# Performance work log

Hardware: AMD Instinct MI355X
Metric: run time of the kernel (lower is better)

## Reference

```python
import jax, jax.numpy as jnp
import numpy as np

NUM_GROUPS = 32
EPS = 1e-5


def group_norm(x, scale, bias):
    # x: [b, c, h, w]
    b, c, h, w = x.shape
    xg = x.reshape(b, NUM_GROUPS, c // NUM_GROUPS, h, w)
    mean = jnp.mean(xg, axis=(2, 3, 4), keepdims=True)
    var = jnp.var(xg, axis=(2, 3, 4), keepdims=True)
    xg = (xg - mean) * jax.lax.rsqrt(var + EPS)
    xn = xg.reshape(b, c, h, w)
    return xn * scale[None, :, None, None] + bias[None, :, None, None]


def conv1x1(x, w, b):
    # x: [b, c_in, h, w], w: [c_out, c_in], b: [c_out]
    return jnp.einsum('bchw,dc->bdhw', x, w) + b[None, :, None, None]


def setup_inputs() -> dict:
    key = jax.random.key(0)
    ks = jax.random.split(key, 11)
    B, C, H, W = 16, 512, 32, 32
    s = 1.0 / np.sqrt(C)
    inp = {
        'x': jax.random.normal(ks[0], (B, C, H, W), jnp.float32),
        'gn_scale': jnp.ones((C,), jnp.float32),
        'gn_bias': jnp.zeros((C,), jnp.float32),
        'wq': jax.random.normal(ks[1], (C, C), jnp.float32) * s,
        'bq': jnp.zeros((C,), jnp.float32),
        'wk': jax.random.normal(ks[2], (C, C), jnp.float32) * s,
        'bk': jnp.zeros((C,), jnp.float32),
        'wv': jax.random.normal(ks[3], (C, C), jnp.float32) * s,
        'bv': jnp.zeros((C,), jnp.float32),
        'wp': jax.random.normal(ks[4], (C, C), jnp.float32) * s,
        'bp': jnp.zeros((C,), jnp.float32),
    }
    return inp


def reference(x, gn_scale, gn_bias, wq, bq, wk, bk, wv, bv, wp, bp):
    b, c, h, w = x.shape
    xn = group_norm(x, gn_scale, gn_bias)
    q = conv1x1(xn, wq, bq).reshape(b, c, h * w)  # [b, c, n]
    k = conv1x1(xn, wk, bk).reshape(b, c, h * w)
    v = conv1x1(xn, wv, bv).reshape(b, c, h * w)
    # attn[b, i, j] = sum_c q[b, c, i] * k[b, c, j]
    attn = jnp.einsum('bci,bcj->bij', q, k) * (c ** -0.5)
    A = jax.nn.softmax(attn, axis=-1)
    # out[b, c, i] = sum_j A[b, i, j] * v[b, c, j]
    out = jnp.einsum('bij,bcj->bci', A, v).reshape(b, c, h, w)
    scores = conv1x1(out, wp, bp)
    return x + scores
```

## Files before the change

kernel.cpp:

```cpp
#include <hip/hip_runtime.h>

typedef __bf16 bf16x8 __attribute__((ext_vector_type(8)));
typedef float  f32x4  __attribute__((ext_vector_type(4)));

__device__ __forceinline__ unsigned short f2bf(float f) {
    union { float f; unsigned int u; } x; x.f = f;
    unsigned int r = (x.u + 0x7FFFu + ((x.u >> 16) & 1u)) >> 16;
    return (unsigned short)r;
}

typedef const __attribute__((address_space(1))) unsigned short gu16;
typedef __attribute__((address_space(3)))       unsigned short lu16;
__device__ __forceinline__ void gl_lds16(const unsigned short* g, unsigned short* l) {
    __builtin_amdgcn_global_load_lds((gu16*)g, (lu16*)l, 16, 0, 0);
}

__device__ __forceinline__ void stage_tiles(
    const unsigned short* __restrict__ Ab, int lda,
    const unsigned short* __restrict__ Bb, int ldb,
    int k0, unsigned short* Ad, unsigned short* Bd,
    int wave, int r0, int c0)
{
    gl_lds16(Ab + (long)r0 * lda + c0 + k0,        Ad + wave * 512);
    gl_lds16(Ab + (long)(r0 + 64) * lda + c0 + k0, Ad + 2048 + wave * 512);
    gl_lds16(Bb + (long)r0 * ldb + c0 + k0,        Bd + wave * 512);
    gl_lds16(Bb + (long)(r0 + 64) * ldb + c0 + k0, Bd + 2048 + wave * 512);
}

__device__ __forceinline__ void gemm_core_db(
    const unsigned short* __restrict__ Ab, int lda,
    const unsigned short* __restrict__ Bb, int ldb,
    int K, f32x4 (&acc)[4][4],
    unsigned short* As, unsigned short* Bs)
{
    const int tid  = threadIdx.x;
    const int lane = tid & 63;
    const int wave = tid >> 6;
    const int wm   = (wave >> 1) * 64;
    const int wn   = (wave & 1) * 64;
    const int l16  = lane & 15;
    const int quad = lane >> 4;

    const int r0 = wave * 16 + (lane >> 2);
    const int c0 = ((lane & 3) ^ ((lane >> 3) & 3)) * 8;

    stage_tiles(Ab, lda, Bb, ldb, 0, As, Bs, wave, r0, c0);

    const int sw8 = ((l16 >> 1) & 3) * 8;

    int sel = 0;
    for (int k0 = 0; k0 < K; k0 += 32) {
        __syncthreads();
        if (k0 + 32 < K)
            stage_tiles(Ab, lda, Bb, ldb, k0 + 32,
                        As + (sel ^ 1) * 4096, Bs + (sel ^ 1) * 4096, wave, r0, c0);

        const unsigned short* Ap = As + sel * 4096;
        const unsigned short* Bp = Bs + sel * 4096;
        bf16x8 af[4], bfr[4];
        #pragma unroll
        for (int mi = 0; mi < 4; mi++)
            af[mi] = *(const bf16x8*)&Ap[(wm + mi * 16 + l16) * 32 + ((quad * 8) ^ sw8)];
        #pragma unroll
        for (int ni = 0; ni < 4; ni++)
            bfr[ni] = *(const bf16x8*)&Bp[(wn + ni * 16 + l16) * 32 + ((quad * 8) ^ sw8)];
        #pragma unroll
        for (int mi = 0; mi < 4; mi++)
            #pragma unroll
            for (int ni = 0; ni < 4; ni++)
                acc[mi][ni] = __builtin_amdgcn_mfma_f32_16x16x32_bf16(af[mi], bfr[ni], acc[mi][ni], 0, 0, 0);
        sel ^= 1;
    }
}

template<typename OutT, bool TRANS_OUT, bool HAS_BIAS, bool HAS_RESID,
         bool EXP_SUM, bool ROW_SCALE>
__global__ __launch_bounds__(256) void gemm_k(
    const unsigned short* __restrict__ Ag, long sA, int lda,
    const unsigned short* __restrict__ Bg, long sB, int ldb,
    OutT* __restrict__ Cg, long sC, int ldc,
    const float* __restrict__ bias,
    const float* __restrict__ resid, long sR,
    float* __restrict__ lsum, long sL,
    float alpha, int K)
{
    __shared__ __align__(16) unsigned short LB[16384];
    unsigned short* As = LB;
    unsigned short* Bs = LB + 8192;

    const unsigned short* Ab = Ag + (long)blockIdx.z * sA + (long)(blockIdx.y * 128) * lda;
    const unsigned short* Bb = Bg + (long)blockIdx.z * sB + (long)(blockIdx.x * 128) * ldb;

    f32x4 acc[4][4] = {};
    gemm_core_db(Ab, lda, Bb, ldb, K, acc, As, Bs);

    const int lane = threadIdx.x & 63;
    const int wave = threadIdx.x >> 6;
    const int l16  = lane & 15;
    const int quad = lane >> 4;
    const int mb = blockIdx.y * 128 + (wave >> 1) * 64;
    const int nb = blockIdx.x * 128 + (wave & 1) * 64;

    if constexpr (sizeof(OutT) == 2) {
        __syncthreads();
        unsigned short* scr = LB + wave * 4096;

        #pragma unroll
        for (int mi = 0; mi < 4; mi++) {
            float rsum[4];
            if constexpr (EXP_SUM) { rsum[0] = rsum[1] = rsum[2] = rsum[3] = 0.f; }
            #pragma unroll
            for (int ni = 0; ni < 4; ni++) {
                f32x4 v = acc[mi][ni];
                float invl;
                if constexpr (ROW_SCALE) invl = 1.f / lsum[(long)blockIdx.z * sL + nb + ni * 16 + l16];
                float o[4];
                #pragma unroll
                for (int r = 0; r < 4; r++) {
                    float val = v[r] * alpha;
                    if constexpr (HAS_BIAS) val += bias[mb + mi * 16 + quad * 4 + r];
                    if constexpr (EXP_SUM) { val = __expf(val); rsum[r] += val; }
                    if constexpr (ROW_SCALE) val *= invl;
                    o[r] = val;
                }
                if constexpr (TRANS_OUT) {
                    const int nl = ni * 16 + l16;
                    const int ch = mi * 2 + (quad >> 1);
                    ushort4 p; p.x = f2bf(o[0]); p.y = f2bf(o[1]); p.z = f2bf(o[2]); p.w = f2bf(o[3]);
                    *(ushort4*)&scr[nl * 64 + ((ch ^ (nl & 7)) * 8) + (quad & 1) * 4] = p;
                } else {
                    #pragma unroll
                    for (int r = 0; r < 4; r++) {
                        const int ml = mi * 16 + quad * 4 + r;
                        const int nc = ni * 2 + (l16 >> 3);
                        scr[ml * 64 + ((nc ^ (ml & 7)) * 8) + (l16 & 7)] = f2bf(o[r]);
                    }
                }
            }
            if constexpr (EXP_SUM) {
                const int m0 = mb + mi * 16 + quad * 4;
                #pragma unroll
                for (int r = 0; r < 4; r++) {
                    float s = rsum[r];
                    s += __shfl_xor(s, 1); s += __shfl_xor(s, 2);
                    s += __shfl_xor(s, 4); s += __shfl_xor(s, 8);
                    if (l16 == 0)
                        atomicAdd(&lsum[(long)blockIdx.z * sL + m0 + r], s);
                }
            }
        }
        __syncthreads();

        const int ch2 = lane & 7;
        const int rr  = lane >> 3;
        unsigned short* Cs = (unsigned short*)Cg + (long)blockIdx.z * sC;
        if constexpr (TRANS_OUT) {
            unsigned short* dst = Cs + mb + ch2 * 8;
            #pragma unroll
            for (int it = 0; it < 8; it++) {
                const int nl = rr + it * 8;
                uint4 v = *(uint4*)&scr[nl * 64 + ((ch2 ^ (nl & 7)) * 8)];
                *(uint4*)(dst + (long)(nb + nl) * ldc) = v;
            }
        } else {
            unsigned short* dst = Cs + nb + ch2 * 8;
            #pragma unroll
            for (int it = 0; it < 8; it++) {
                const int ml = rr + it * 8;
                uint4 v = *(uint4*)&scr[ml * 64 + ((ch2 ^ (ml & 7)) * 8)];
                *(uint4*)(dst + (long)(mb + ml) * ldc) = v;
            }
        }
    } else {
        #pragma unroll
        for (int mi = 0; mi < 4; mi++) {
            #pragma unroll
            for (int ni = 0; ni < 4; ni++) {
                f32x4 v = acc[mi][ni];
                const int m0 = mb + mi * 16 + quad * 4;
                const int n  = nb + ni * 16 + l16;
                const long base = (long)blockIdx.z * sC;
                #pragma unroll
                for (int r = 0; r < 4; r++) {
                    float val = v[r] * alpha;
                    if (HAS_BIAS) val += bias[m0 + r];
                    if (HAS_RESID) val += resid[(long)blockIdx.z * sR + (long)(m0 + r) * ldc + n];
                    ((float*)Cg)[base + (long)(m0 + r) * ldc + n] = val;
                }
            }
        }
    }
}

__global__ __launch_bounds__(256) void qkv_k(
    const unsigned short* __restrict__ Wqkv,
    const unsigned short* __restrict__ xnT,
    unsigned short* __restrict__ qT,
    unsigned short* __restrict__ kT,
    unsigned short* __restrict__ vB,
    const float* __restrict__ bqkv)
{
    __shared__ __align__(16) unsigned short LB[16384];
    unsigned short* As = LB;
    unsigned short* Bs = LB + 8192;

    const unsigned short* Ab = Wqkv + (long)(blockIdx.y * 128) * 512;
    const unsigned short* Bb = xnT + (long)blockIdx.z * 524288 + (long)(blockIdx.x * 128) * 512;

    f32x4 acc[4][4] = {};
    gemm_core_db(Ab, 512, Bb, 512, 512, acc, As, Bs);

    const int lane = threadIdx.x & 63;
    const int wave = threadIdx.x >> 6;
    const int l16  = lane & 15;
    const int quad = lane >> 4;
    const int mb = blockIdx.y * 128 + (wave >> 1) * 64;
    const int nb = blockIdx.x * 128 + (wave & 1) * 64;
    const int mat = blockIdx.y >> 2;
    const long zb = (long)blockIdx.z * 524288;

    __syncthreads();
    unsigned short* scr = LB + wave * 4096;

    #pragma unroll
    for (int mi = 0; mi < 4; mi++) {
        #pragma unroll
        for (int ni = 0; ni < 4; ni++) {
            f32x4 v = acc[mi][ni];
            const int m0 = mb + mi * 16 + quad * 4;
            float o[4];
            #pragma unroll
            for (int r = 0; r < 4; r++) o[r] = v[r] + bqkv[m0 + r];
            if (mat == 2) {
                #pragma unroll
                for (int r = 0; r < 4; r++) {
                    const int ml = mi * 16 + quad * 4 + r;
                    const int nc = ni * 2 + (l16 >> 3);
                    scr[ml * 64 + ((nc ^ (ml & 7)) * 8) + (l16 & 7)] = f2bf(o[r]);
                }
            } else {
                const int nl = ni * 16 + l16;
                const int ch = mi * 2 + (quad >> 1);
                ushort4 p; p.x = f2bf(o[0]); p.y = f2bf(o[1]); p.z = f2bf(o[2]); p.w = f2bf(o[3]);
                *(ushort4*)&scr[nl * 64 + ((ch ^ (nl & 7)) * 8) + (quad & 1) * 4] = p;
            }
        }
    }
    __syncthreads();

    const int ch2 = lane & 7;
    const int rr  = lane >> 3;
    const int ml0 = mb & 511;
    if (mat == 2) {
        unsigned short* dst = vB + zb + nb + ch2 * 8;
        #pragma unroll
        for (int it = 0; it < 8; it++) {
            const int ml = rr + it * 8;
            uint4 v = *(uint4*)&scr[ml * 64 + ((ch2 ^ (ml & 7)) * 8)];
            *(uint4*)(dst + (long)(ml0 + ml) * 1024) = v;
        }
    } else {
        unsigned short* dst = ((mat == 0) ? qT : kT) + zb + ml0 + ch2 * 8;
        #pragma unroll
        for (int it = 0; it < 8; it++) {
            const int nl = rr + it * 8;
            uint4 v = *(uint4*)&scr[nl * 64 + ((ch2 ^ (nl & 7)) * 8)];
            *(uint4*)(dst + (long)(nb + nl) * 512) = v;
        }
    }
}

__global__ __launch_bounds__(256) void gn_k(
    const float* __restrict__ x, const float* __restrict__ gsc,
    const float* __restrict__ gbi, unsigned short* __restrict__ xnT)
{
    __shared__ __align__(16) unsigned short ln[16 * 1024];
    __shared__ float red[8];
    const int b = blockIdx.y, g = blockIdx.x;
    const int tid = threadIdx.x, lane = tid & 63, wv = tid >> 6;

    const float4* x4 = (const float4*)(x + ((long)b * 512 + g * 16) * 1024);
    float4 vals[16];
    float s = 0.f, ss = 0.f;
    #pragma unroll
    for (int i = 0; i < 16; i++) {
        float4 v = x4[tid + i * 256];
        vals[i] = v;
        s  += v.x + v.y + v.z + v.w;
        ss += v.x * v.x + v.y * v.y + v.z * v.z + v.w * v.w;
    }
    for (int o = 32; o; o >>= 1) { s += __shfl_down(s, o); ss += __shfl_down(ss, o); }
    if (lane == 0) { red[wv * 2] = s; red[wv * 2 + 1] = ss; }
    __syncthreads();
    const float S  = red[0] + red[2] + red[4] + red[6];
    const float SS = red[1] + red[3] + red[5] + red[7];
    const float mean = S * (1.f / 16384.f);
    const float var  = SS * (1.f / 16384.f) - mean * mean;
    const float inv  = rsqrtf(var + 1e-5f);

    #pragma unroll
    for (int i = 0; i < 16; i++) {
        const int idx = tid + i * 256;
        const int c   = idx >> 8;
        const float sc = gsc[g * 16 + c] * inv;
        const float bi = gbi[g * 16 + c] - mean * sc;
        float4 v = vals[i];
        ushort4 p;
        p.x = f2bf(v.x * sc + bi); p.y = f2bf(v.y * sc + bi);
        p.z = f2bf(v.z * sc + bi); p.w = f2bf(v.w * sc + bi);
        ((ushort4*)ln)[idx] = p;
    }
    __syncthreads();

    unsigned short* op = xnT + (long)b * 1024 * 512 + g * 16;
    for (int rep = 0; rep < 4; rep++) {
        const int n = rep * 256 + tid;
        union { unsigned short u[16]; uint4 v[2]; } t;
        #pragma unroll
        for (int c = 0; c < 16; c++) t.u[c] = ln[c * 1024 + n];
        *(uint4*)&op[(long)n * 512]     = t.v[0];
        *(uint4*)&op[(long)n * 512 + 8] = t.v[1];
    }
}

__global__ __launch_bounds__(256) void wconv_k(
    const float* __restrict__ w0, const float* __restrict__ w1,
    const float* __restrict__ w2, const float* __restrict__ w3,
    const float* __restrict__ b0, const float* __restrict__ b1,
    const float* __restrict__ b2,
    unsigned short* __restrict__ out, float* __restrict__ bqkv,
    float* __restrict__ lsum)
{
    const int m = blockIdx.y;
    const int i = blockIdx.x * 256 + threadIdx.x;
    if (m == 4) {
        if (i < 384) {
            const int which = i >> 7, off = i & 127;
            const float* src = (which == 0) ? b0 : (which == 1) ? b1 : b2;
            ((float4*)bqkv)[i] = ((const float4*)src)[off];
        }
        if (i < 16384) lsum[i] = 0.f;
        return;
    }
    const float* src = (m == 0) ? w0 : (m == 1) ? w1 : (m == 2) ? w2 : w3;
    float4 v = ((const float4*)src)[i];
    ushort4 o; o.x = f2bf(v.x); o.y = f2bf(v.y); o.z = f2bf(v.z); o.w = f2bf(v.w);
    ((ushort4*)(out + (long)m * 262144))[i] = o;
}

extern "C" void kernel_launch(void* const* d_in, const int* in_sizes, int n_in,
                              void* d_out, int out_size, void* d_ws, size_t ws_size,
                              hipStream_t stream)
{
    const float* x   = (const float*)d_in[0];
    const float* gsc = (const float*)d_in[1];
    const float* gbi = (const float*)d_in[2];
    const float* wq  = (const float*)d_in[3];
    const float* bq  = (const float*)d_in[4];
    const float* wk  = (const float*)d_in[5];
    const float* bk  = (const float*)d_in[6];
    const float* wv  = (const float*)d_in[7];
    const float* bv  = (const float*)d_in[8];
    const float* wp  = (const float*)d_in[9];
    const float* bp  = (const float*)d_in[10];
    float* out = (float*)d_out;

    char* ws = (char*)d_ws;
    unsigned short* xnT = (unsigned short*)(ws);
    unsigned short* qT  = (unsigned short*)(ws + 16777216);
    unsigned short* kT  = (unsigned short*)(ws + 33554432);
    unsigned short* vB  = (unsigned short*)(ws + 50331648);
    unsigned short* Sb  = (unsigned short*)(ws + 67108864);
    unsigned short* Wb  = (unsigned short*)(ws + 100663296);
    float*          bqkv= (float*)        (ws + 102760448);
    float*          Lb  = (float*)        (ws + 102768640);
    unsigned short* OT  = xnT;

    const long sBCN = 512L * 1024;

    wconv_k<<<dim3(256, 5), 256, 0, stream>>>(wq, wk, wv, wp, bq, bk, bv, Wb, bqkv, Lb);
    gn_k<<<dim3(32, 16), 256, 0, stream>>>(x, gsc, gbi, xnT);

    qkv_k<<<dim3(8, 12, 16), 256, 0, stream>>>(Wb, xnT, qT, kT, vB, bqkv);

    gemm_k<unsigned short, false, false, false, true, false>
        <<<dim3(8, 8, 16), 256, 0, stream>>>(
        qT, sBCN, 512, kT, sBCN, 512, Sb, 1048576L, 1024, nullptr, nullptr, 0,
        Lb, 1024, 0.044194173824159216f, 512);

    gemm_k<unsigned short, true, false, false, false, true>
        <<<dim3(8, 4, 16), 256, 0, stream>>>(
        vB, sBCN, 1024, Sb, 1048576L, 1024, OT, sBCN, 512,
        nullptr, nullptr, 0, Lb, 1024, 1.f, 1024);

    gemm_k<float, false, true, true, false, false>
        <<<dim3(8, 4, 16), 256, 0, stream>>>(
        Wb + 786432, 0, 512, OT, sBCN, 512, out, sBCN, 1024, bp, x, sBCN,
        nullptr, 0, 1.f, 512);
}
```

Before: 225.9 us.

## Use 256x256-tile 8-wave pipelined GEMM core for QKV and score kernels

Adds a new GEMM core with 256x256 output tiles per 512-thread block, a 128KB LDS multi-buffer with interleaved global-to-LDS staging, explicit barriers/waitcnts and priority hints around MFMA clusters. QKV projection and QK^T score kernels are rewritten on top of it, with fused exp/row-sum epilogue and swizzled LDS transpose for stores. Larger tiles raise arithmetic intensity and reduce redundant global loads, but reduce grid size (fewer blocks than CUs for some launches) and increase register/LDS pressure.

After: 224.4 us. Within noise of the previous version (-0.6%).

```diff
diff --git a/kernel.cpp b/kernel.cpp
--- a/kernel.cpp
+++ b/kernel.cpp
@@ -13,6 +13,258 @@
 typedef __attribute__((address_space(3)))       unsigned short lu16;
 __device__ __forceinline__ void gl_lds16(const unsigned short* g, unsigned short* l) {
     __builtin_amdgcn_global_load_lds((gu16*)g, (lu16*)l, 16, 0, 0);
+}
+
+__device__ __forceinline__ void stage8(
+    const unsigned short* __restrict__ Ab, int lda,
+    const unsigned short* __restrict__ Bb, int ldb,
+    unsigned short* LB, int s, int s_max, int wave, int lane)
+{
+    if (s >= s_max) return;
+    const int tau  = s >> 2;
+    const int pi   = s & 3;
+    const int isA  = pi >> 1;
+    const int half = pi & 1;
+    unsigned short* dst = LB + (isA ? 0 : 32768) + (tau & 1) * 16384 + half * 8192 + wave * 512;
+    const unsigned short* src = isA ? Ab : Bb;
+    const int ld = isA ? lda : ldb;
+    const int R  = half * 128 + wave * 8 + (lane >> 3);
+    const int kc = tau * 64 + (((lane & 7) ^ ((lane >> 5) << 1)) << 3);
+    gl_lds16(src + (long)R * ld + kc,        dst);
+    gl_lds16(src + (long)(R + 64) * ld + kc, dst + 4096);
+}
+
+template<int NT>
+__device__ __forceinline__ void gemm8_core(
+    const unsigned short* __restrict__ Ab, int lda,
+    const unsigned short* __restrict__ Bb, int ldb,
+    f32x4 (&acc)[8][4], unsigned short* LB)
+{
+    const int tid  = threadIdx.x;
+    const int lane = tid & 63;
+    const int wave = tid >> 6;
+    const int wM   = wave >> 2;
+    const int wN   = wave & 3;
+    const int l16  = lane & 15;
+    const int quad = lane >> 4;
+    const int ckx  = quad ^ (((l16 >> 2) & 1) << 1);
+    const int aoff = wM * 8192 + l16 * 64 + ckx * 8;
+    const int boff = 32768 + (wN >> 1) * 8192 + ((wN & 1) * 64 + l16) * 64 + ckx * 8;
+
+    #pragma unroll
+    for (int s = 0; s < 7; ++s)
+        stage8(Ab, lda, Bb, ldb, LB, s, 4 * NT, wave, lane);
+    asm volatile("s_waitcnt vmcnt(6)" ::: "memory");
+    __builtin_amdgcn_s_barrier();
+    __builtin_amdgcn_sched_barrier(0);
+
+    bf16x8 af[4][2], bf[4][2];
+
+#define RD_A(buf, mh)                                                         \
+    _Pragma("unroll")                                                         \
+    for (int m = 0; m < 4; ++m)                                               \
+        _Pragma("unroll")                                                     \
+        for (int kk = 0; kk < 2; ++kk)                                        \
+            af[m][kk] = *(const bf16x8*)&LB[(buf) * 16384 + aoff + ((mh) * 4 + m) * 1024 + kk * 32];
+#define RD_B(buf)                                                             \
+    _Pragma("unroll")                                                         \
+    for (int n = 0; n < 4; ++n)                                               \
+        _Pragma("unroll")                                                     \
+        for (int kk = 0; kk < 2; ++kk)                                        \
+            bf[n][kk] = *(const bf16x8*)&LB[(buf) * 16384 + boff + n * 1024 + kk * 32];
+#define MF(mh, nh)                                                            \
+    __builtin_amdgcn_s_setprio(1);                                            \
+    _Pragma("unroll")                                                         \
+    for (int m = 0; m < 4; ++m)                                               \
+        _Pragma("unroll")                                                     \
+        for (int n = 0; n < 2; ++n)                                           \
+            _Pragma("unroll")                                                 \
+            for (int kk = 0; kk < 2; ++kk)                                    \
+                acc[(mh)*4+m][(nh)*2+n] = __builtin_amdgcn_mfma_f32_16x16x32_bf16( \
+                    af[m][kk], bf[(nh)*2+n][kk], acc[(mh)*4+m][(nh)*2+n], 0, 0, 0); \
+    __builtin_amdgcn_s_setprio(0);
+#define BARS do { __builtin_amdgcn_s_barrier(); __builtin_amdgcn_sched_barrier(0); } while (0)
+#define LGW  do { asm volatile("s_waitcnt lgkmcnt(0)" ::: "memory"); __builtin_amdgcn_sched_barrier(0); } while (0)
+
+    const int NITER = NT / 2;
+    for (int i = 0; i < NITER; ++i) {
+        const int s0 = 6 + 8 * i;
+        RD_B(0) RD_A(0, 0)
+        stage8(Ab, lda, Bb, ldb, LB, s0 + 1, 4 * NT, wave, lane);
+        BARS; LGW;
+        MF(0, 0)
+        BARS;
+        stage8(Ab, lda, Bb, ldb, LB, s0 + 2, 4 * NT, wave, lane);
+        BARS;
+        MF(0, 1)
+        BARS;
+        RD_A(0, 1)
+        stage8(Ab, lda, Bb, ldb, LB, s0 + 3, 4 * NT, wave, lane);
+        BARS; LGW;
+        MF(1, 0)
+        BARS;
+        stage8(Ab, lda, Bb, ldb, LB, s0 + 4, 4 * NT, wave, lane);
+        BARS;
+        MF(1, 1)
+        if (i == NITER - 1) { asm volatile("s_waitcnt vmcnt(0)" ::: "memory"); }
+        else                { asm volatile("s_waitcnt vmcnt(6)" ::: "memory"); }
+        BARS;
+        RD_B(1) RD_A(1, 0)
+        stage8(Ab, lda, Bb, ldb, LB, s0 + 5, 4 * NT, wave, lane);
+        BARS; LGW;
+        MF(0, 0)
+        BARS;
+        stage8(Ab, lda, Bb, ldb, LB, s0 + 6, 4 * NT, wave, lane);
+        BARS;
+        MF(0, 1)
+        BARS;
+        RD_A(1, 1)
+        stage8(Ab, lda, Bb, ldb, LB, s0 + 7, 4 * NT, wave, lane);
+        BARS; LGW;
+        MF(1, 0)
+        BARS;
+        stage8(Ab, lda, Bb, ldb, LB, s0 + 8, 4 * NT, wave, lane);
+        BARS;
+        MF(1, 1)
+        if (i < NITER - 1) { asm volatile("s_waitcnt vmcnt(6)" ::: "memory"); }
+        BARS;
+    }
+#undef RD_A
+#undef RD_B
+#undef MF
+#undef BARS
+#undef LGW
+}
+
+__global__ __launch_bounds__(512, 2) void p8_k(
+    const unsigned short* __restrict__ qT,
+    const unsigned short* __restrict__ kT,
+    unsigned short* __restrict__ Sb,
+    float* __restrict__ lsum,
+    float alpha)
+{
+    __shared__ __align__(16) unsigned short LB[65536];
+    const int z = blockIdx.z;
+    const unsigned short* Ab = qT + (long)z * 524288 + (long)(blockIdx.y * 256) * 512;
+    const unsigned short* Bb = kT + (long)z * 524288 + (long)(blockIdx.x * 256) * 512;
+    f32x4 acc[8][4] = {};
+    gemm8_core<8>(Ab, 512, Bb, 512, acc, LB);
+
+    const int lane = threadIdx.x & 63, wave = threadIdx.x >> 6;
+    const int wM = wave >> 2, wN = wave & 3;
+    const int l16 = lane & 15, quad = lane >> 4;
+    const int gm0 = blockIdx.y * 256 + wM * 128;
+    const int gn0 = blockIdx.x * 256 + wN * 64;
+    unsigned short* scr = LB + wave * 8192;
+
+    float rs[8][4];
+    #pragma unroll
+    for (int mi = 0; mi < 8; ++mi) { rs[mi][0] = rs[mi][1] = rs[mi][2] = rs[mi][3] = 0.f; }
+    #pragma unroll
+    for (int mi = 0; mi < 8; ++mi)
+        #pragma unroll
+        for (int ni = 0; ni < 4; ++ni) {
+            f32x4 v = acc[mi][ni];
+            #pragma unroll
+            for (int r = 0; r < 4; ++r) {
+                float e = __expf(v[r] * alpha);
+                rs[mi][r] += e;
+                const int row = mi * 16 + quad * 4 + r;
+                const int col = ni * 16 + l16;
+                scr[row * 64 + (((col >> 3) ^ (row & 7)) << 3) + (col & 7)] = f2bf(e);
+            }
+        }
+    #pragma unroll
+    for (int mi = 0; mi < 8; ++mi)
+        #pragma unroll
+        for (int r = 0; r < 4; ++r) {
+            float s = rs[mi][r];
+            s += __shfl_xor(s, 1); s += __shfl_xor(s, 2);
+            s += __shfl_xor(s, 4); s += __shfl_xor(s, 8);
+            if (l16 == 0)
+                atomicAdd(&lsum[(long)z * 1024 + gm0 + mi * 16 + quad * 4 + r], s);
+        }
+    unsigned short* dst = Sb + (long)z * 1048576;
+    #pragma unroll
+    for (int it = 0; it < 16; ++it) {
+        const int row = it * 8 + (lane >> 3);
+        const int ck  = lane & 7;
+        uint4 vv = *(uint4*)&scr[row * 64 + ((ck ^ (row & 7)) << 3)];
+        *(uint4*)&dst[(long)(gm0 + row) * 1024 + gn0 + ck * 8] = vv;
+    }
+}
+
+__global__ __launch_bounds__(512, 2) void qkv8_k(
+    const unsigned short* __restrict__ Wqkv,
+    const unsigned short* __restrict__ xnT,
+    unsigned short* __restrict__ qT,
+    unsigned short* __restrict__ kT,
+    unsigned short* __restrict__ vB,
+    const float* __restrict__ bqkv)
+{
+    __shared__ __align__(16) unsigned short LB[65536];
+    const int z = blockIdx.z;
+    const unsigned short* Ab = Wqkv + (long)(blockIdx.y * 256) * 512;
+    const unsigned short* Bb = xnT + (long)z * 524288 + (long)(blockIdx.x * 256) * 512;
+    f32x4 acc[8][4] = {};
+    gemm8_core<8>(Ab, 512, Bb, 512, acc, LB);
+
+    const int lane = threadIdx.x & 63, wave = threadIdx.x >> 6;
+    const int wM = wave >> 2, wN = wave & 3;
+    const int l16 = lane & 15, quad = lane >> 4;
+    const int gm0 = blockIdx.y * 256 + wM * 128;
+    const int gn0 = blockIdx.x * 256 + wN * 64;
+    const int mat = blockIdx.y >> 1;
+    const int ml0 = gm0 & 511;
+    const long zb = (long)z * 524288;
+    unsigned short* scr = LB + wave * 8192;
+
+    if (mat == 2) {
+        #pragma unroll
+        for (int mi = 0; mi < 8; ++mi)
+            #pragma unroll
+            for (int ni = 0; ni < 4; ++ni) {
+                f32x4 v = acc[mi][ni];
+                #pragma unroll
+                for (int r = 0; r < 4; ++r) {
+                    const int row = mi * 16 + quad * 4 + r;
+                    const int col = ni * 16 + l16;
+                    scr[row * 64 + (((col >> 3) ^ (row & 7)) << 3) + (col & 7)] =
+                        f2bf(v[r] + bqkv[gm0 + row]);
+                }
+            }
+        #pragma unroll
+        for (int it = 0; it < 16; ++it) {
+            const int row = it * 8 + (lane >> 3);
+            const int ck  = lane & 7;
+            uint4 vv = *(uint4*)&scr[row * 64 + ((ck ^ (row & 7)) << 3)];
+            *(uint4*)&vB[zb + (long)(ml0 + row) * 1024 + gn0 + ck * 8] = vv;
+        }
+    } else {
+        unsigned short* dstm = (mat == 0) ? qT : kT;
+        #pragma unroll
+        for (int mi = 0; mi < 8; ++mi)
+            #pragma unroll
+            for (int ni = 0; ni < 4; ++ni) {
+                f32x4 v = acc[mi][ni];
+                const int nl = ni * 16 + l16;
+                const int ch = mi * 2 + (quad >> 1);
+                const int m4 = gm0 + mi * 16 + quad * 4;
+                ushort4 p;
+                p.x = f2bf(v[0] + bqkv[m4 + 0]);
+                p.y = f2bf(v[1] + bqkv[m4 + 1]);
+                p.z = f2bf(v[2] + bqkv[m4 + 2]);
+                p.w = f2bf(v[3] + bqkv[m4 + 3]);
+                *(ushort4*)&scr[nl * 128 + ((ch ^ (nl & 15)) << 3) + (quad & 1) * 4] = p;
+            }
+        #pragma unroll
+        for (int it = 0; it < 16; ++it) {
+            const int nl  = it * 4 + (lane >> 4);
+            const int chl = lane & 15;
+            uint4 vv = *(uint4*)&scr[nl * 128 + ((chl ^ (nl & 15)) << 3)];
+            *(uint4*)&dstm[zb + (long)(gn0 + nl) * 512 + ml0 + chl * 8] = vv;
+        }
+    }
 }
 
 __device__ __forceinline__ void stage_tiles(
@@ -192,84 +444,6 @@
     }
 }
 
-__global__ __launch_bounds__(256) void qkv_k(
-    const unsigned short* __restrict__ Wqkv,
-    const unsigned short* __restrict__ xnT,
-    unsigned short* __restrict__ qT,
-    unsigned short* __restrict__ kT,
-    unsigned short* __restrict__ vB,
-    const float* __restrict__ bqkv)
-{
-    __shared__ __align__(16) unsigned short LB[16384];
-    unsigned short* As = LB;
-    unsigned short* Bs = LB + 8192;
-
-    const unsigned short* Ab = Wqkv + (long)(blockIdx.y * 128) * 512;
-    const unsigned short* Bb = xnT + (long)blockIdx.z * 524288 + (long)(blockIdx.x * 128) * 512;
-
-    f32x4 acc[4][4] = {};
-    gemm_core_db(Ab, 512, Bb, 512, 512, acc, As, Bs);
-
-    const int lane = threadIdx.x & 63;
-    const int wave = threadIdx.x >> 6;
-    const int l16  = lane & 15;
-    const int quad = lane >> 4;
-    const int mb = blockIdx.y * 128 + (wave >> 1) * 64;
-    const int nb = blockIdx.x * 128 + (wave & 1) * 64;
-    const int mat = blockIdx.y >> 2;
-    const long zb = (long)blockIdx.z * 524288;
-
-    __syncthreads();
-    unsigned short* scr = LB + wave * 4096;
-
-    #pragma unroll
-    for (int mi = 0; mi < 4; mi++) {
-        #pragma unroll
-        for (int ni = 0; ni < 4; ni++) {
-            f32x4 v = acc[mi][ni];
-            const int m0 = mb + mi * 16 + quad * 4;
-            float o[4];
-            #pragma unroll
-            for (int r = 0; r < 4; r++) o[r] = v[r] + bqkv[m0 + r];
-            if (mat == 2) {
-                #pragma unroll
-                for (int r = 0; r < 4; r++) {
-                    const int ml = mi * 16 + quad * 4 + r;
-                    const int nc = ni * 2 + (l16 >> 3);
-                    scr[ml * 64 + ((nc ^ (ml & 7)) * 8) + (l16 & 7)] = f2bf(o[r]);
-                }
-            } else {
-                const int nl = ni * 16 + l16;
-                const int ch = mi * 2 + (quad >> 1);
-                ushort4 p; p.x = f2bf(o[0]); p.y = f2bf(o[1]); p.z = f2bf(o[2]); p.w = f2bf(o[3]);
-                *(ushort4*)&scr[nl * 64 + ((ch ^ (nl & 7)) * 8) + (quad & 1) * 4] = p;
-            }
-        }
-    }
-    __syncthreads();
-
-    const int ch2 = lane & 7;
-    const int rr  = lane >> 3;
-    const int ml0 = mb & 511;
-    if (mat == 2) {
-        unsigned short* dst = vB + zb + nb + ch2 * 8;
-        #pragma unroll
-        for (int it = 0; it < 8; it++) {
-            const int ml = rr + it * 8;
-            uint4 v = *(uint4*)&scr[ml * 64 + ((ch2 ^ (ml & 7)) * 8)];
-            *(uint4*)(dst + (long)(ml0 + ml) * 1024) = v;
-        }
-    } else {
-        unsigned short* dst = ((mat == 0) ? qT : kT) + zb + ml0 + ch2 * 8;
-        #pragma unroll
-        for (int it = 0; it < 8; it++) {
-            const int nl = rr + it * 8;
-            uint4 v = *(uint4*)&scr[nl * 64 + ((ch2 ^ (nl & 7)) * 8)];
-            *(uint4*)(dst + (long)(nb + nl) * 512) = v;
-        }
-    }
-}
-
 __global__ __launch_bounds__(256) void gn_k(
     const float* __restrict__ x, const float* __restrict__ gsc,
     const float* __restrict__ gbi, unsigned short* __restrict__ xnT)
@@ -381,12 +555,9 @@
     wconv_k<<<dim3(256, 5), 256, 0, stream>>>(wq, wk, wv, wp, bq, bk, bv, Wb, bqkv, Lb);
     gn_k<<<dim3(32, 16), 256, 0, stream>>>(x, gsc, gbi, xnT);
 
-    qkv_k<<<dim3(8, 12, 16), 256, 0, stream>>>(Wb, xnT, qT, kT, vB, bqkv);
-
-    gemm_k<unsigned short, false, false, false, true, false>
-        <<<dim3(8, 8, 16), 256, 0, stream>>>(
-        qT, sBCN, 512, kT, sBCN, 512, Sb, 1048576L, 1024, nullptr, nullptr, 0,
-        Lb, 1024, 0.044194173824159216f, 512);
+    qkv8_k<<<dim3(4, 6, 16), 512, 0, stream>>>(Wb, xnT, qT, kT, vB, bqkv);
+
+    p8_k<<<dim3(4, 4, 16), 512, 0, stream>>>(qT, kT, Sb, Lb, 0.044194173824159216f);
 
     gemm_k<unsigned short, true, false, false, false, true>
         <<<dim3(8, 4, 16), 256, 0, stream>>>(
```
